# Kernel optimization log

Hardware: AMD Instinct MI355X
Metric: run time of the kernel (lower is better)

## Reference

```python
import jax, jax.numpy as jnp
import numpy as np

EMBED = 512
HIDDEN = 512
VOCAB = 32000
NUM_LAYERS = 2
BATCH = 32
SEQ = 64


def setup_inputs() -> dict:
    key = jax.random.key(0)
    ks = jax.random.split(key, 16)
    s_in = 1.0 / np.sqrt(EMBED + HIDDEN)  # torch Linear default U(-1/sqrt(fan_in), ..)
    s_h = 1.0 / np.sqrt(HIDDEN)
    s_e = 1.0 / np.sqrt(EMBED)
    u = lambda k, shape, s: jax.random.uniform(k, shape, jnp.float32, -s, s)
    # gate weights stacked over layers; both layers have in_dim = 1024 since embed==hidden
    gw = lambda k: u(k, (NUM_LAYERS, HIDDEN, EMBED + HIDDEN), s_in)
    gb = lambda k: u(k, (NUM_LAYERS, HIDDEN), s_in)
    return {
        "features": jax.random.normal(ks[0], (BATCH, EMBED), jnp.float32),
        "captions": jax.random.randint(ks[1], (BATCH, SEQ), 0, VOCAB),
        "embedding_w": jax.random.normal(ks[2], (VOCAB, EMBED), jnp.float32),
        "Wf": gw(ks[3]), "bf": gb(ks[4]),
        "Wi": gw(ks[5]), "bi": gb(ks[6]),
        "Wc": gw(ks[7]), "bc": gb(ks[8]),
        "Wo": gw(ks[9]), "bo": gb(ks[10]),
        "out_w": u(ks[11], (VOCAB, HIDDEN), s_h),
        "out_b": u(ks[12], (VOCAB,), s_h),
        "init_h_w": u(ks[13], (HIDDEN, EMBED), s_e),
        "init_h_b": u(ks[13], (HIDDEN,), s_e),
        "init_c_w": u(ks[14], (HIDDEN, EMBED), s_e),
        "init_c_b": u(ks[14], (HIDDEN,), s_e),
    }


def reference(features, captions, embedding_w, Wf, bf, Wi, bi, Wc, bc, Wo, bo,
              out_w, out_b, init_h_w, init_h_b, init_c_w, init_c_b):
    # init hidden/cell states (same projection replicated to every layer)
    h0 = features @ init_h_w.T + init_h_b           # [B, H]
    c0 = features @ init_c_w.T + init_c_b
    h = jnp.broadcast_to(h0, (NUM_LAYERS,) + h0.shape)  # [L, B, H]
    c = jnp.broadcast_to(c0, (NUM_LAYERS,) + c0.shape)

    # embeddings for captions[:, :-1]; dropout = identity (eval mode)
    emb = embedding_w[captions[:, :-1]]             # [B, T, E]
    xs = jnp.swapaxes(emb, 0, 1)                    # [T, B, E]

    def step(carry, x_t):
        h, c = carry
        for l in range(NUM_LAYERS):
            comb = jnp.concatenate([x_t, h[l]], axis=1)  # [B, E+H]
            f_t = jax.nn.sigmoid(comb @ Wf[l].T + bf[l])
            i_t = jax.nn.sigmoid(comb @ Wi[l].T + bi[l])
            o_t = jax.nn.sigmoid(comb @ Wo[l].T + bo[l])
            c_til = jnp.tanh(comb @ Wc[l].T + bc[l])
            c_new = f_t * c[l] + i_t * c_til
            h_new = o_t * jnp.tanh(c_new)
            h = h.at[l].set(h_new)
            c = c.at[l].set(c_new)
            x_t = h_new
        logits = h[-1] @ out_w.T + out_b            # [B, V]
        return (h, c), logits

    (_, _), outs = jax.lax.scan(step, (h, c), xs)   # outs: [T, B, V]
    return jnp.swapaxes(outs, 0, 1)                 # [B, T, V]
```

## Files before the change

kernel.cpp:

```cpp
#include <hip/hip_runtime.h>
#include <hip/hip_bf16.h>

#define T_STEPS 63
#define BATCHSZ 32
#define HID 512
#define VOCAB 32000
#define HSZ (BATCHSZ * HID)

typedef __bf16 bf16x8 __attribute__((ext_vector_type(8)));
typedef float f32x4 __attribute__((ext_vector_type(4)));

__device__ __forceinline__ unsigned short f2bf(float f) {
    __hip_bfloat16 h = __float2bfloat16(f);
    return *reinterpret_cast<unsigned short*>(&h);
}
__device__ __forceinline__ float sigm(float x) { return 1.0f / (1.0f + __expf(-x)); }

__device__ __forceinline__ float4 coh16(const float* p) {
    const unsigned long long* q = reinterpret_cast<const unsigned long long*>(p);
    unsigned long long a = __hip_atomic_load(q,     __ATOMIC_RELAXED, __HIP_MEMORY_SCOPE_AGENT);
    unsigned long long b = __hip_atomic_load(q + 1, __ATOMIC_RELAXED, __HIP_MEMORY_SCOPE_AGENT);
    float4 v;
    v.x = __uint_as_float((unsigned)(a & 0xffffffffu));
    v.y = __uint_as_float((unsigned)(a >> 32));
    v.z = __uint_as_float((unsigned)(b & 0xffffffffu));
    v.w = __uint_as_float((unsigned)(b >> 32));
    return v;
}
__device__ __forceinline__ void coh_store(float* p, float v) {
    __hip_atomic_store(p, v, __ATOMIC_RELAXED, __HIP_MEMORY_SCOPE_AGENT);
}

__device__ __forceinline__ void grid_barrier(unsigned* bar, int bid, unsigned step) {
    __syncthreads();
    const int tid = threadIdx.x;
    if (tid == 0)
        __hip_atomic_store(&bar[bid], step, __ATOMIC_RELAXED, __HIP_MEMORY_SCOPE_AGENT);
    if (tid < 64) {
        const unsigned* f = bar + tid;
        for (;;) {
            unsigned a = __hip_atomic_load(f,       __ATOMIC_RELAXED, __HIP_MEMORY_SCOPE_AGENT);
            unsigned b = __hip_atomic_load(f + 64,  __ATOMIC_RELAXED, __HIP_MEMORY_SCOPE_AGENT);
            unsigned c = __hip_atomic_load(f + 128, __ATOMIC_RELAXED, __HIP_MEMORY_SCOPE_AGENT);
            unsigned d = __hip_atomic_load(f + 192, __ATOMIC_RELAXED, __HIP_MEMORY_SCOPE_AGENT);
            if (__all(a >= step && b >= step && c >= step && d >= step)) break;
            __builtin_amdgcn_s_sleep(1);
        }
        asm volatile("" ::: "memory");
    }
    __syncthreads();
}

__global__ __launch_bounds__(512, 1) void lstm_persistent(
    const float* __restrict__ feat, const int* __restrict__ caps,
    const float* __restrict__ emb,
    const float* __restrict__ Wf, const float* __restrict__ bfp,
    const float* __restrict__ Wi, const float* __restrict__ bip,
    const float* __restrict__ Wc, const float* __restrict__ bcp,
    const float* __restrict__ Wo, const float* __restrict__ bop,
    const float* __restrict__ ihw, const float* __restrict__ ihb,
    const float* __restrict__ icw, const float* __restrict__ icb,
    float* h0buf, float* h1buf, unsigned short* h1all, unsigned* bar)
{
    __shared__ float comb[16 * 1024];
    __shared__ float red[8 * 32 * 20];

    const int tid = threadIdx.x;
    const int bid = blockIdx.x;
    const int l   = bid >> 7;
    const int sub = bid & 127;
    const int j0  = (sub >> 1) << 3;
    const int b0  = (sub & 1) << 4;

    const int wv  = tid >> 6;
    const int seg = (wv << 2) | ((tid >> 4) & 3);
    const int rl  = tid & 15;
    const int g   = rl >> 3;
    const int u   = rl & 7;

    const int cg   = tid & 255;
    const int bhi  = tid >> 8;
    const int slotW = cg ^ ((cg >> 3) & 7);
    const int chOff = (cg < 128) ? cg : (cg - 128);

    float4* comb4 = reinterpret_cast<float4*>(comb);
    const float4* emb4 = reinterpret_cast<const float4*>(emb);

    const float* WgA = (g == 0) ? Wf : Wi;
    const float* WgB = (g == 0) ? Wc : Wo;
    const float4* rowA4 = reinterpret_cast<const float4*>(
        WgA + ((size_t)((l << 9) + j0 + u) << 10));
    const float4* rowB4 = reinterpret_cast<const float4*>(
        WgB + ((size_t)((l << 9) + j0 + u) << 10));
    float4 w4A[8], w4B[8];
    #pragma unroll
    for (int q = 0; q < 8; ++q) {
        w4A[q] = rowA4[(seg << 3) + q];
        w4B[q] = rowB4[(seg << 3) + q];
    }

    float c_reg = 0.f, bf_r = 0.f, bi_r = 0.f, bc_r = 0.f, bo_r = 0.f;
    if (tid < 128) {
        const int uu = tid >> 4, bc = tid & 15;
        const int j = j0 + uu, b = b0 + bc;
        bf_r = bfp[(l << 9) + j];
        bi_r = bip[(l << 9) + j];
        bc_r = bcp[(l << 9) + j];
        bo_r = bop[(l << 9) + j];
        const float4* fr = reinterpret_cast<const float4*>(feat + ((size_t)b << 9));
        const float4* hr = reinterpret_cast<const float4*>(ihw + ((size_t)j << 9));
        const float4* cr = reinterpret_cast<const float4*>(icw + ((size_t)j << 9));
        float sh = 0.f, sc = 0.f;
        #pragma unroll 4
        for (int k = 0; k < 128; ++k) {
            float4 f = fr[k], hv = hr[k], cv = cr[k];
            sh += f.x * hv.x + f.y * hv.y + f.z * hv.z + f.w * hv.w;
            sc += f.x * cv.x + f.y * cv.y + f.z * cv.z + f.w * cv.w;
        }
        sh += ihb[j];
        c_reg = sc + icb[j];
        float* hb = (l == 0 ? h0buf : h1buf) + HSZ;
        coh_store(&hb[((size_t)b << 9) + j], sh);
    }

    float4 pf[8];
    if (l == 0 && cg < 128) {
        #pragma unroll
        for (int k = 0; k < 8; ++k) {
            int b = b0 + (k << 1) + bhi;
            int tok = caps[b << 6];
            pf[k] = emb4[(size_t)tok * 128 + cg];
        }
    }

    grid_barrier(bar, bid, 1u);

    for (int s = 0; s < 64; ++s) {
        const bool active = (l == 0) ? (s < 63) : (s >= 1);
        if (active) {
            const int t = (l == 0) ? s : (s - 1);
            const float* h0p = h0buf + (((s + 1) & 1) ? HSZ : 0);
            const float* h1p = h1buf + ((s & 1) ? HSZ : 0);
            const bool fromPf = (l == 0 && cg < 128);
            const float* src = (l == 0) ? h0p : ((cg < 128) ? h0p : h1p);

            {
                float4 L0, L1;
                if (!fromPf) {
                    L0 = coh16(src + ((size_t)(b0 + bhi)     << 9) + (chOff << 2));
                    L1 = coh16(src + ((size_t)(b0 + 2 + bhi) << 9) + (chOff << 2));
                }
                if (fromPf) {
                    comb4[(bhi)     * 256 + slotW] = pf[0];
                    comb4[(2 + bhi) * 256 + slotW] = pf[1];
                } else {
                    comb4[(bhi)     * 256 + slotW] = L0;
                    comb4[(2 + bhi) * 256 + slotW] = L1;
                }
            }
            __syncthreads();

            #pragma unroll
            for (int c = 0; c < 4; ++c) {
                float4 L0, L1;
                if (c < 3 && !fromPf) {
                    L0 = coh16(src + ((size_t)(b0 + 4*(c+1) + bhi)     << 9) + (chOff << 2));
                    L1 = coh16(src + ((size_t)(b0 + 4*(c+1) + 2 + bhi) << 9) + (chOff << 2));
                }
                float aA[4], aB[4];
                #pragma unroll
                for (int bi2 = 0; bi2 < 4; ++bi2) {
                    const float4* cb = comb4 + (4*c + bi2) * 256;
                    float sA0 = 0.f, sA1 = 0.f, sB0 = 0.f, sB1 = 0.f;
                    #pragma unroll
                    for (int q = 0; q < 8; ++q) {
                        float4 cc = cb[(seg << 3) | (q ^ (seg & 7))];
                        sA0 += w4A[q].x*cc.x + w4A[q].y*cc.y;
                        sA1 += w4A[q].z*cc.z + w4A[q].w*cc.w;
                        sB0 += w4B[q].x*cc.x + w4B[q].y*cc.y;
                        sB1 += w4B[q].z*cc.z + w4B[q].w*cc.w;
                    }
                    aA[bi2] = sA0 + sA1;
                    aB[bi2] = sB0 + sB1;
                }
                #pragma unroll
                for (int bi2 = 0; bi2 < 4; ++bi2) {
                    aA[bi2] += __shfl_down(aA[bi2], 16);
                    aB[bi2] += __shfl_down(aB[bi2], 16);
                    aA[bi2] += __shfl_down(aA[bi2], 32);
                    aB[bi2] += __shfl_down(aB[bi2], 32);
                }
                if ((tid & 63) < 16) {
                    *reinterpret_cast<float4*>(
                        &red[((wv << 5) + rl) * 20 + (c << 2)]) =
                        make_float4(aA[0], aA[1], aA[2], aA[3]);
                    *reinterpret_cast<float4*>(
                        &red[((wv << 5) + rl + 16) * 20 + (c << 2)]) =
                        make_float4(aB[0], aB[1], aB[2], aB[3]);
                }
                if (c < 3) {
                    if (fromPf) {
                        comb4[(4*(c+1) + bhi)     * 256 + slotW] = pf[2*(c+1)];
                        comb4[(4*(c+1) + 2 + bhi) * 256 + slotW] = pf[2*(c+1) + 1];
                    } else {
                        comb4[(4*(c+1) + bhi)     * 256 + slotW] = L0;
                        comb4[(4*(c+1) + 2 + bhi) * 256 + slotW] = L1;
                    }
                }
                __syncthreads();
            }

            if (l == 0 && cg < 128 && s < 62) {
                #pragma unroll
                for (int k = 0; k < 8; ++k) {
                    int b = b0 + (k << 1) + bhi;
                    int tok = caps[(b << 6) + s + 1];
                    pf[k] = emb4[(size_t)tok * 128 + cg];
                }
            }

            if (tid < 128) {
                const int uu = tid >> 4, bc = tid & 15;
                const int j = j0 + uu, b = b0 + bc;
                float s0 = 0.f, s1 = 0.f, s2 = 0.f, s3 = 0.f;
                #pragma unroll
                for (int w = 0; w < 8; ++w) {
                    s0 += red[((w << 5) + uu)      * 20 + bc];
                    s1 += red[((w << 5) + 8 + uu)  * 20 + bc];
                    s2 += red[((w << 5) + 16 + uu) * 20 + bc];
                    s3 += red[((w << 5) + 24 + uu) * 20 + bc];
                }
                float fg = sigm(s0 + bf_r), ig = sigm(s1 + bi_r);
                float ct = tanhf(s2 + bc_r), og = sigm(s3 + bo_r);
                float cn = fg * c_reg + ig * ct;
                c_reg = cn;
                float hn = og * tanhf(cn);
                if (l == 0) {
                    coh_store(&h0buf[(s & 1) * HSZ + ((size_t)b << 9) + j], hn);
                } else {
                    coh_store(&h1buf[((s + 1) & 1) * HSZ + ((size_t)b << 9) + j], hn);
                    h1all[((size_t)b * 63 + t) * 512 + j] = f2bf(hn);
                }
            }
        }
        if (s < 63) grid_barrier(bar, bid, (unsigned)(s + 2));
    }
}

__global__ __launch_bounds__(256) void proj_gemm(
    const unsigned short* __restrict__ H, const float* __restrict__ W,
    const float* __restrict__ bias, float* __restrict__ out)
{
    __shared__ unsigned short sA[128 * 72];
    __shared__ unsigned short sB[128 * 72];
    const int tid = threadIdx.x;
    const int bm = blockIdx.x, bn = blockIdx.y;
    const int wave = tid >> 6, lane = tid & 63;
    const int wm = (wave >> 1) << 6, wn = (wave & 1) << 6;
    const int lr = lane & 15, quad = lane >> 4;

    f32x4 acc[4][4];
    #pragma unroll
    for (int i = 0; i < 4; ++i)
        #pragma unroll
        for (int j = 0; j < 4; ++j) acc[i][j] = (f32x4){0.f, 0.f, 0.f, 0.f};

    for (int k0 = 0; k0 < 512; k0 += 64) {
        __syncthreads();
        #pragma unroll
        for (int it = 0; it < 4; ++it) {
            int c = tid + (it << 8);
            int row = c >> 3, col = (c & 7) << 3;
            int gm = (bm << 7) + row;
            uint4 av = make_uint4(0u, 0u, 0u, 0u);
            if (gm < 2016)
                av = *reinterpret_cast<const uint4*>(&H[(size_t)gm * 512 + k0 + col]);
            *reinterpret_cast<uint4*>(&sA[row * 72 + col]) = av;
        }
        #pragma unroll
        for (int it = 0; it < 8; ++it) {
            int c = tid + (it << 8);
            int row = c >> 4, col = (c & 15) << 2;
            int gn = (bn << 7) + row;
            float4 bv = *reinterpret_cast<const float4*>(&W[(size_t)gn * 512 + k0 + col]);
            uint2 p;
            p.x = (unsigned int)f2bf(bv.x) | ((unsigned int)f2bf(bv.y) << 16);
            p.y = (unsigned int)f2bf(bv.z) | ((unsigned int)f2bf(bv.w) << 16);
            *reinterpret_cast<uint2*>(&sB[row * 72 + col]) = p;
        }
        __syncthreads();
        #pragma unroll
        for (int ks = 0; ks < 2; ++ks) {
            bf16x8 af[4], bg[4];
            #pragma unroll
            for (int i = 0; i < 4; ++i)
                af[i] = *reinterpret_cast<const bf16x8*>(
                    &sA[(wm + (i << 4) + lr) * 72 + (ks << 5) + (quad << 3)]);
            #pragma unroll
            for (int i = 0; i < 4; ++i)
                bg[i] = *reinterpret_cast<const bf16x8*>(
                    &sB[(wn + (i << 4) + lr) * 72 + (ks << 5) + (quad << 3)]);
            #pragma unroll
            for (int mi = 0; mi < 4; ++mi)
                #pragma unroll
                for (int ni = 0; ni < 4; ++ni)
                    acc[mi][ni] = __builtin_amdgcn_mfma_f32_16x16x32_bf16(
                        af[mi], bg[ni], acc[mi][ni], 0, 0, 0);
        }
    }

    #pragma unroll
    for (int ni = 0; ni < 4; ++ni) {
        int n = (bn << 7) + wn + (ni << 4) + lr;
        float bv = bias[n];
        #pragma unroll
        for (int mi = 0; mi < 4; ++mi) {
            #pragma unroll
            for (int r = 0; r < 4; ++r) {
                int m = (bm << 7) + wm + (mi << 4) + (quad << 2) + r;
                if (m < 2016)
                    out[(size_t)m * VOCAB + n] = acc[mi][ni][r] + bv;
            }
        }
    }
}

extern "C" void kernel_launch(void* const* d_in, const int* in_sizes, int n_in,
                              void* d_out, int out_size, void* d_ws, size_t ws_size,
                              hipStream_t stream) {
    const float* feat = (const float*)d_in[0];
    const int*   caps = (const int*)d_in[1];
    const float* emb  = (const float*)d_in[2];
    const float* Wf   = (const float*)d_in[3];
    const float* bfp  = (const float*)d_in[4];
    const float* Wi   = (const float*)d_in[5];
    const float* bip  = (const float*)d_in[6];
    const float* Wc   = (const float*)d_in[7];
    const float* bcp  = (const float*)d_in[8];
    const float* Wo   = (const float*)d_in[9];
    const float* bop  = (const float*)d_in[10];
    const float* Wout = (const float*)d_in[11];
    const float* bout = (const float*)d_in[12];
    const float* ihw  = (const float*)d_in[13];
    const float* ihb  = (const float*)d_in[14];
    const float* icw  = (const float*)d_in[15];
    const float* icb  = (const float*)d_in[16];

    char* ws = (char*)d_ws;
    unsigned* bar         = (unsigned*)ws;
    float* h0buf          = (float*)(ws + 1024);
    float* h1buf          = (float*)(ws + 1024 + 131072);
    unsigned short* h1all = (unsigned short*)(ws + 1024 + 262144);

    hipMemsetAsync(ws, 0, 1024, stream);

    lstm_persistent<<<dim3(256), dim3(512), 0, stream>>>(
        feat, caps, emb, Wf, bfp, Wi, bip, Wc, bcp, Wo, bop,
        ihw, ihb, icw, icb, h0buf, h1buf, h1all, bar);

    proj_gemm<<<dim3(16, 250), dim3(256), 0, stream>>>(h1all, Wout, bout,
                                                       (float*)d_out);
}
```

Measured before the change: 1.596 ms.

## Restructure LSTM gate matvec: four gates per thread, single staging pass, LDS reduction

Each thread now holds weights for all four gates of one unit and segment, and the two batch halves are split across waves. The old design held two gates per thread and processed the batch in four chunks with shuffle reductions and a barrier per chunk. The full comb tile is now staged in one pass, then every thread writes per-segment partial sums to LDS, and 128 threads reduce 32 segments. This removes the per-chunk __syncthreads and cross-lane shuffles. In exchange it doubles weight register use, uses more LDS, and no longer overlaps the global h loads with compute.

```diff
diff --git a/kernel.cpp b/kernel.cpp
--- a/kernel.cpp
+++ b/kernel.cpp
@@ -1,5 +1,6 @@
 #include <hip/hip_runtime.h>
 #include <hip/hip_bf16.h>
+#include <stdint.h>
 
 #define T_STEPS 63
 #define BATCHSZ 32
@@ -62,8 +63,8 @@
     const float* __restrict__ icw, const float* __restrict__ icb,
     float* h0buf, float* h1buf, unsigned short* h1all, unsigned* bar)
 {
-    __shared__ float comb[16 * 1024];
-    __shared__ float red[8 * 32 * 20];
+    __shared__ alignas(128) float4 comb4[4096];
+    __shared__ alignas(128) float4 red4[4096];
 
     const int tid = threadIdx.x;
     const int bid = blockIdx.x;
@@ -72,32 +73,27 @@
     const int j0  = (sub >> 1) << 3;
     const int b0  = (sub & 1) << 4;
 
-    const int wv  = tid >> 6;
-    const int seg = (wv << 2) | ((tid >> 4) & 3);
-    const int rl  = tid & 15;
-    const int g   = rl >> 3;
-    const int u   = rl & 7;
-
-    const int cg   = tid & 255;
-    const int bhi  = tid >> 8;
+    const int lane = tid & 63;
+    const int u    = lane & 7;
+    const int sl   = lane >> 3;
+    const int wv   = tid >> 6;
+    const int bg   = wv & 1;
+    const int seg  = ((wv >> 1) << 3) | sl;
+    const int sx   = seg & 7;
+
+    const int cg    = tid & 255;
+    const int bhi   = tid >> 8;
     const int slotW = cg ^ ((cg >> 3) & 7);
-    const int chOff = (cg < 128) ? cg : (cg - 128);
-
-    float4* comb4 = reinterpret_cast<float4*>(comb);
-    const float4* emb4 = reinterpret_cast<const float4*>(emb);
-
-    const float* WgA = (g == 0) ? Wf : Wi;
-    const float* WgB = (g == 0) ? Wc : Wo;
-    const float4* rowA4 = reinterpret_cast<const float4*>(
-        WgA + ((size_t)((l << 9) + j0 + u) << 10));
-    const float4* rowB4 = reinterpret_cast<const float4*>(
-        WgB + ((size_t)((l << 9) + j0 + u) << 10));
-    float4 w4A[8], w4B[8];
+    const bool xpf  = (l == 0) && (cg < 128);
+
+    const size_t rowOff = ((size_t)((l << 9) + j0 + u)) << 10;
+    const float4* f4 = reinterpret_cast<const float4*>(Wf + rowOff) + (seg << 3);
+    const float4* i4 = reinterpret_cast<const float4*>(Wi + rowOff) + (seg << 3);
+    const float4* c4 = reinterpret_cast<const float4*>(Wc + rowOff) + (seg << 3);
+    const float4* o4 = reinterpret_cast<const float4*>(Wo + rowOff) + (seg << 3);
+    float4 wF[8], wI[8], wC[8], wO[8];
     #pragma unroll
-    for (int q = 0; q < 8; ++q) {
-        w4A[q] = rowA4[(seg << 3) + q];
-        w4B[q] = rowB4[(seg << 3) + q];
-    }
+    for (int q = 0; q < 8; ++q) { wF[q]=f4[q]; wI[q]=i4[q]; wC[q]=c4[q]; wO[q]=o4[q]; }
 
     float c_reg = 0.f, bf_r = 0.f, bi_r = 0.f, bc_r = 0.f, bo_r = 0.f;
     if (tid < 128) {
@@ -123,16 +119,15 @@
         coh_store(&hb[((size_t)b << 9) + j], sh);
     }
 
-    float4 pf[8];
-    if (l == 0 && cg < 128) {
+    float4 stg[8];
+    if (xpf) {
         #pragma unroll
         for (int k = 0; k < 8; ++k) {
-            int b = b0 + (k << 1) + bhi;
-            int tok = caps[b << 6];
-            pf[k] = emb4[(size_t)tok * 128 + cg];
-        }
-    }
-
+            int bR = (k << 1) + bhi;
+            int tok = caps[(b0 + bR) << 6];
+            stg[k] = reinterpret_cast<const float4*>(emb)[(size_t)tok * 128 + cg];
+        }
+    }
     grid_barrier(bar, bid, 1u);
 
     for (int s = 0; s < 64; ++s) {
@@ -141,97 +136,65 @@
             const int t = (l == 0) ? s : (s - 1);
             const float* h0p = h0buf + (((s + 1) & 1) ? HSZ : 0);
             const float* h1p = h1buf + ((s & 1) ? HSZ : 0);
-            const bool fromPf = (l == 0 && cg < 128);
-            const float* src = (l == 0) ? h0p : ((cg < 128) ? h0p : h1p);
+
+            if (!xpf) {
+                const float* src = (l == 1 && cg >= 128) ? h1p : h0p;
+                const int co = (cg & 127) << 2;
+                #pragma unroll
+                for (int k = 0; k < 8; ++k) {
+                    int bR = (k << 1) + bhi;
+                    stg[k] = coh16(src + (((size_t)(b0 + bR)) << 9) + co);
+                }
+            }
+            #pragma unroll
+            for (int k = 0; k < 8; ++k)
+                comb4[(((k << 1) + bhi) << 8) + slotW] = stg[k];
+            __syncthreads();
 
             {
-                float4 L0, L1;
-                if (!fromPf) {
-                    L0 = coh16(src + ((size_t)(b0 + bhi)     << 9) + (chOff << 2));
-                    L1 = coh16(src + ((size_t)(b0 + 2 + bhi) << 9) + (chOff << 2));
-                }
-                if (fromPf) {
-                    comb4[(bhi)     * 256 + slotW] = pf[0];
-                    comb4[(2 + bhi) * 256 + slotW] = pf[1];
-                } else {
-                    comb4[(bhi)     * 256 + slotW] = L0;
-                    comb4[(2 + bhi) * 256 + slotW] = L1;
-                }
-            }
-            __syncthreads();
-
-            #pragma unroll
-            for (int c = 0; c < 4; ++c) {
-                float4 L0, L1;
-                if (c < 3 && !fromPf) {
-                    L0 = coh16(src + ((size_t)(b0 + 4*(c+1) + bhi)     << 9) + (chOff << 2));
-                    L1 = coh16(src + ((size_t)(b0 + 4*(c+1) + 2 + bhi) << 9) + (chOff << 2));
-                }
-                float aA[4], aB[4];
-                #pragma unroll
-                for (int bi2 = 0; bi2 < 4; ++bi2) {
-                    const float4* cb = comb4 + (4*c + bi2) * 256;
-                    float sA0 = 0.f, sA1 = 0.f, sB0 = 0.f, sB1 = 0.f;
+                const float4* crb = comb4 + (bg << 11) + (seg << 3);
+                #pragma unroll
+                for (int b = 0; b < 8; ++b) {
+                    uintptr_t base = reinterpret_cast<uintptr_t>(crb + (b << 8))
+                                   | (uintptr_t)((unsigned)(sx << 4));
+                    float f0=0.f,f1=0.f,i0=0.f,i1=0.f;
+                    float c0=0.f,c1=0.f,o0=0.f,o1=0.f;
                     #pragma unroll
                     for (int q = 0; q < 8; ++q) {
-                        float4 cc = cb[(seg << 3) | (q ^ (seg & 7))];
-                        sA0 += w4A[q].x*cc.x + w4A[q].y*cc.y;
-                        sA1 += w4A[q].z*cc.z + w4A[q].w*cc.w;
-                        sB0 += w4B[q].x*cc.x + w4B[q].y*cc.y;
-                        sB1 += w4B[q].z*cc.z + w4B[q].w*cc.w;
+                        float4 cc = *reinterpret_cast<const float4*>(
+                                        base ^ (uintptr_t)((unsigned)(q << 4)));
+                        f0 += wF[q].x*cc.x + wF[q].y*cc.y;  f1 += wF[q].z*cc.z + wF[q].w*cc.w;
+                        i0 += wI[q].x*cc.x + wI[q].y*cc.y;  i1 += wI[q].z*cc.z + wI[q].w*cc.w;
+                        c0 += wC[q].x*cc.x + wC[q].y*cc.y;  c1 += wC[q].z*cc.z + wC[q].w*cc.w;
+                        o0 += wO[q].x*cc.x + wO[q].y*cc.y;  o1 += wO[q].z*cc.z + wO[q].w*cc.w;
                     }
-                    aA[bi2] = sA0 + sA1;
-                    aB[bi2] = sB0 + sB1;
-                }
-                #pragma unroll
-                for (int bi2 = 0; bi2 < 4; ++bi2) {
-                    aA[bi2] += __shfl_down(aA[bi2], 16);
-                    aB[bi2] += __shfl_down(aB[bi2], 16);
-                    aA[bi2] += __shfl_down(aA[bi2], 32);
-                    aB[bi2] += __shfl_down(aB[bi2], 32);
-                }
-                if ((tid & 63) < 16) {
-                    *reinterpret_cast<float4*>(
-                        &red[((wv << 5) + rl) * 20 + (c << 2)]) =
-                        make_float4(aA[0], aA[1], aA[2], aA[3]);
-                    *reinterpret_cast<float4*>(
-                        &red[((wv << 5) + rl + 16) * 20 + (c << 2)]) =
-                        make_float4(aB[0], aB[1], aB[2], aB[3]);
-                }
-                if (c < 3) {
-                    if (fromPf) {
-                        comb4[(4*(c+1) + bhi)     * 256 + slotW] = pf[2*(c+1)];
-                        comb4[(4*(c+1) + 2 + bhi) * 256 + slotW] = pf[2*(c+1) + 1];
-                    } else {
-                        comb4[(4*(c+1) + bhi)     * 256 + slotW] = L0;
-                        comb4[(4*(c+1) + 2 + bhi) * 256 + slotW] = L1;
-                    }
-                }
-                __syncthreads();
-            }
-
-            if (l == 0 && cg < 128 && s < 62) {
+                    red4[(bg << 11) + (seg << 6) + (u << 3) + (b ^ u)] =
+                        make_float4(f0 + f1, i0 + i1, c0 + c1, o0 + o1);
+                }
+            }
+            __syncthreads();
+
+            if (xpf && s < 62) {
                 #pragma unroll
                 for (int k = 0; k < 8; ++k) {
-                    int b = b0 + (k << 1) + bhi;
-                    int tok = caps[(b << 6) + s + 1];
-                    pf[k] = emb4[(size_t)tok * 128 + cg];
+                    int bR = (k << 1) + bhi;
+                    int tok = caps[((b0 + bR) << 6) + s + 1];
+                    stg[k] = reinterpret_cast<const float4*>(emb)[(size_t)tok * 128 + cg];
                 }
             }
 
             if (tid < 128) {
                 const int uu = tid >> 4, bc = tid & 15;
                 const int j = j0 + uu, b = b0 + bc;
-                float s0 = 0.f, s1 = 0.f, s2 = 0.f, s3 = 0.f;
-                #pragma unroll
-                for (int w = 0; w < 8; ++w) {
-                    s0 += red[((w << 5) + uu)      * 20 + bc];
-                    s1 += red[((w << 5) + 8 + uu)  * 20 + bc];
-                    s2 += red[((w << 5) + 16 + uu) * 20 + bc];
-                    s3 += red[((w << 5) + 24 + uu) * 20 + bc];
-                }
-                float fg = sigm(s0 + bf_r), ig = sigm(s1 + bi_r);
-                float ct = tanhf(s2 + bc_r), og = sigm(s3 + bo_r);
+                const float4* rr = red4 + ((bc >> 3) << 11) + (uu << 3) + ((bc & 7) ^ uu);
+                float sfv = 0.f, siv = 0.f, scv = 0.f, sov = 0.f;
+                #pragma unroll
+                for (int s2 = 0; s2 < 32; ++s2) {
+                    float4 v = rr[s2 << 6];
+                    sfv += v.x; siv += v.y; scv += v.z; sov += v.w;
+                }
+                float fg = sigm(sfv + bf_r), ig = sigm(siv + bi_r);
+                float ct = tanhf(scv + bc_r), og = sigm(sov + bo_r);
                 float cn = fg * c_reg + ig * ct;
                 c_reg = cn;
                 float hn = og * tanhf(cn);
```

Measured after the change: 2.912 ms. 82.5% more time.
